# Performance work log

Hardware: AMD Instinct MI355X
Metric: run time of the kernel (lower is better)

The kernel has to match this reference:

```python
import jax, jax.numpy as jnp
import numpy as np

EPSILON = float(np.finfo(np.float32).tiny)
K = 32                 # self.k
TRAIN_ENSEMBLE = 2     # repeat_sample in train mode
TAU = 0.1


def setup_inputs() -> dict:
    key = jax.random.key(0)
    scores = jax.random.normal(key, (256, 8192, 4), dtype=jnp.float32)  # [bsz, Nmax, ensemble]
    return {"scores": scores}


def reference(scores):
    bsz, Nmax, ensemble = scores.shape
    repeat = TRAIN_ENSEMBLE
    local_k = min(K, Nmax)

    # flat_scores: (bsz*ensemble, Nmax), then repeated over samples -> (repeat*bsz*ensemble, Nmax)
    flat = scores.transpose(0, 2, 1).reshape(bsz * ensemble, Nmax)
    flat = jnp.tile(flat, (repeat, 1))

    # Gumbel(0,1) noise (m.sample())
    g = jax.random.gumbel(jax.random.key(42), flat.shape, dtype=flat.dtype)
    flat = flat + g

    zeros = jnp.zeros_like(flat)

    def step(carry, _):
        f, khot, onehot = carry
        khot_mask = jnp.maximum(1.0 - onehot, EPSILON)
        f = f + jnp.log(khot_mask)
        onehot = jax.nn.softmax(f / TAU, axis=1)
        return (f, khot + onehot, onehot), None

    (_, khot, _), _ = jax.lax.scan(step, (flat, zeros, zeros), None, length=local_k)

    # hard top-k straight-through
    _, ind = jax.lax.top_k(khot, local_k)                      # (R, local_k)
    rows = jnp.arange(khot.shape[0])[:, None]
    khot_hard = jnp.zeros_like(khot).at[rows, ind].set(1.0)
    res = khot_hard - jax.lax.stop_gradient(khot) + khot

    # (repeat, bsz, ensemble, Nmax) -> (repeat, bsz, Nmax, ensemble)
    new_mask = res.reshape(repeat, bsz, ensemble, Nmax).transpose(0, 1, 3, 2)
    return new_mask
```

## Files before the change

kernel.cpp:

```cpp
#include <hip/hip_runtime.h>

#define TPB 256
#define ROWN 8192
#define CMAX 1024
#define EPS_TINY 1.1754943508222875e-38f

__device__ __forceinline__ unsigned rotl32(unsigned x, int r) {
  return (x << r) | (x >> (32 - r));
}

__device__ __forceinline__ unsigned tf_pxor(unsigned idx) {
  const unsigned ks0 = 0u, ks1 = 42u, ks2 = 0x1BD11BDAu ^ 0u ^ 42u;
  unsigned x0 = ks0;
  unsigned x1 = idx + ks1;
#define TF4(a,b,cc,d) \
  x0 += x1; x1 = rotl32(x1,(a));  x1 ^= x0; \
  x0 += x1; x1 = rotl32(x1,(b));  x1 ^= x0; \
  x0 += x1; x1 = rotl32(x1,(cc)); x1 ^= x0; \
  x0 += x1; x1 = rotl32(x1,(d));  x1 ^= x0;
  TF4(13,15,26,6)   x0 += ks1; x1 += ks2 + 1u;
  TF4(17,29,16,24)  x0 += ks2; x1 += ks0 + 2u;
  TF4(13,15,26,6)   x0 += ks0; x1 += ks1 + 3u;
  TF4(17,29,16,24)  x0 += ks1; x1 += ks2 + 4u;
  TF4(13,15,26,6)   x0 += ks2; x1 += ks0 + 5u;
#undef TF4
  return x0 ^ x1;
}

__device__ __forceinline__ float gumbel_of(unsigned idx) {
  const unsigned bits = tf_pxor(idx);
  float u = __uint_as_float((bits >> 9) | 0x3f800000u) - 1.0f;
  u = u + EPS_TINY;
  u = fmaxf(EPS_TINY, u);
  return -logf(-logf(u));
}

__device__ __forceinline__ float approx_gumbel(unsigned bits) {
  float u = __uint_as_float((bits >> 9) | 0x3f800000u) - 1.0f;
  u = u + EPS_TINY;
  u = fmaxf(EPS_TINY, u);
  float t;
  if (u >= 0.75f) {
    const float v = 1.0f - u;
    t = v * (1.0f + v * (0.5f + v * (0.33333334f + v * (0.25f + v * 0.2f))));
  } else {
    t = -0.69314718f * __log2f(u);
  }
  return -0.69314718f * __log2f(t);
}

__device__ __forceinline__ unsigned key16_of(float x) {
  const unsigned b = __float_as_uint(x) >> 16;
  return (b & 0x8000u) ? (0xFFFFu & ~b) : (b | 0x8000u);
}

__global__ __launch_bounds__(TPB, 8)
void topk_row(const void* __restrict__ scores_raw,
              float* __restrict__ khotArr,
              unsigned short* __restrict__ idxArr,
              int* __restrict__ cntArr,
              float4* __restrict__ out4) {
  const int t    = threadIdx.x;
  const int lane = t & 63;
  const int wave = t >> 6;

  const int i   = blockIdx.x;
  const int xcd = i & 7;
  const int k   = i >> 3;
  const int e   = k & 3;
  const int q   = k >> 2;
  const int b   = xcd * 32 + (q & 31);
  const int rep = q >> 5;
  const int r   = rep * 1024 + b * 4 + e;
  const unsigned gbase = (unsigned)r * (unsigned)ROWN;

  __shared__ unsigned       kLds[16][TPB];
  __shared__ unsigned short candIdx[CMAX];
  __shared__ float redM[2][4];
  __shared__ float redZ[2][4];
  __shared__ int   wtot[13][4];
  __shared__ int   f32flag;

  if (t == 0) f32flag = 0;
  __syncthreads();
  {
    const unsigned* w = (const unsigned*)scores_raw;
    bool bad = false;
#pragma unroll
    for (int p = 0; p < 4; ++p) {
      const unsigned x = w[t + 256 * p];
      const float flo = __uint_as_float((x & 0xFFFFu) << 16);
      const float fhi = __uint_as_float(x & 0xFFFF0000u);
      if (!(fabsf(flo) <= 16.0f) || !(fabsf(fhi) <= 16.0f)) bad = true;
    }
    if (bad) f32flag = 1;
  }

  {
    float4 z; z.x = 0.0f; z.y = 0.0f; z.z = 0.0f; z.w = 0.0f;
    float4* ob = out4 + (size_t)i * 2048;
#pragma unroll
    for (int p = 0; p < 8; ++p) ob[t + 256 * p] = z;
  }
  __syncthreads();
  const bool in_f32 = (f32flag != 0);

  const size_t ebase0 = ((size_t)b * ROWN + (size_t)t) * 4 + (size_t)e;
  float m = -3.4e38f;
  {
    unsigned pair = 0u;
    if (in_f32) {
      const float* sp = (const float*)scores_raw;
#pragma unroll
      for (int j = 0; j < 32; ++j) {
        const float fj = sp[ebase0 + (size_t)(256 * j) * 4]
                       + approx_gumbel(tf_pxor(gbase + (unsigned)(t + 256 * j)));
        m = fmaxf(m, fj);
        const unsigned kk = key16_of(fj);
        if (j & 1) { pair |= kk << 16; kLds[j >> 1][t] = pair; }
        else pair = kk;
      }
    } else {
      const unsigned short* sp = (const unsigned short*)scores_raw;
#pragma unroll
      for (int j = 0; j < 32; ++j) {
        const float fj = __uint_as_float(((unsigned)sp[ebase0 + (size_t)(256 * j) * 4]) << 16)
                       + approx_gumbel(tf_pxor(gbase + (unsigned)(t + 256 * j)));
        m = fmaxf(m, fj);
        const unsigned kk = key16_of(fj);
        if (j & 1) { pair |= kk << 16; kLds[j >> 1][t] = pair; }
        else pair = kk;
      }
    }
  }

#pragma unroll
  for (int off = 32; off >= 1; off >>= 1) m = fmaxf(m, __shfl_xor(m, off));
  if (lane == 0) redM[0][wave] = m;
  __syncthreads();
  m = fmaxf(fmaxf(redM[0][0], redM[0][1]), fmaxf(redM[0][2], redM[0][3]));

  float lo = m - 25.0f, hi = m;
#pragma unroll 1
  for (int itb = 0; itb < 7; ++itb) {
    const float mid = 0.5f * (lo + hi);
    const unsigned kmid = key16_of(mid);
    int c = 0;
#pragma unroll
    for (int h = 0; h < 16; ++h) {
      const unsigned w = kLds[h][t];
      c += ((w & 0xFFFFu) > kmid) ? 1 : 0;
      c += ((w >> 16) > kmid) ? 1 : 0;
    }
#pragma unroll
    for (int off = 32; off >= 1; off >>= 1) c += __shfl_xor(c, off);
    if (lane == 0) wtot[itb][wave] = c;
    __syncthreads();
    const int tot = wtot[itb][0] + wtot[itb][1] + wtot[itb][2] + wtot[itb][3];
    if (tot >= 33) lo = mid; else hi = mid;
  }
  const float theta = lo - 2.34f;
  const unsigned ktheta = key16_of(theta);

  int cj = 0;
#pragma unroll
  for (int h = 0; h < 16; ++h) {
    const unsigned w = kLds[h][t];
    cj += ((w & 0xFFFFu) >= ktheta) ? 1 : 0;
    cj += ((w >> 16) >= ktheta) ? 1 : 0;
  }
  int incv = cj;
#pragma unroll
  for (int off = 1; off < 64; off <<= 1) {
    const int v = __shfl_up(incv, off);
    if (lane >= off) incv += v;
  }
  if (lane == 63) wtot[12][wave] = incv;
  __syncthreads();
  int base = 0;
  for (int w = 0; w < wave; ++w) base += wtot[12][w];
  int cnt = wtot[12][0] + wtot[12][1] + wtot[12][2] + wtot[12][3];
  if (cnt > CMAX) cnt = CMAX;
  int o = base + incv - cj;
#pragma unroll
  for (int h = 0; h < 16; ++h) {
    const unsigned w = kLds[h][t];
    if ((w & 0xFFFFu) >= ktheta) {
      if (o < CMAX) candIdx[o] = (unsigned short)(t + 256 * (2 * h));
      ++o;
    }
    if ((w >> 16) >= ktheta) {
      if (o < CMAX) candIdx[o] = (unsigned short)(t + 256 * (2 * h + 1));
      ++o;
    }
  }
  __syncthreads();

  float cfr[4], khr[4];
#pragma unroll
  for (int p = 0; p < 4; ++p) {
    cfr[p] = -3.0e38f; khr[p] = -3.0e38f;
    if (256 * p < cnt) {
      const int ci = t + 256 * p;
      if (ci < cnt) {
        const int n = (int)candIdx[ci];
        const size_t ei = ((size_t)b * ROWN + (size_t)n) * 4 + (size_t)e;
        float sc;
        if (in_f32) sc = ((const float*)scores_raw)[ei];
        else sc = __uint_as_float(((unsigned)((const unsigned short*)scores_raw)[ei]) << 16);
        cfr[p] = sc + gumbel_of(gbase + (unsigned)n);
        khr[p] = 0.0f;
      }
    }
  }

  float m2;
  {
    float mm = -3.4e38f;
#pragma unroll
    for (int p = 0; p < 4; ++p)
      if (256 * p < cnt) mm = fmaxf(mm, cfr[p]);
#pragma unroll
    for (int off = 32; off >= 1; off >>= 1) mm = fmaxf(mm, __shfl_xor(mm, off));
    if (lane == 0) redM[1][wave] = mm;
    __syncthreads();
    m2 = fmaxf(fmaxf(redM[1][0], redM[1][1]), fmaxf(redM[1][2], redM[1][3]));
  }

#pragma unroll 1
  for (int it = 0; it < 32; ++it) {
    float ek[4];
    float Z = 0.0f;
#pragma unroll
    for (int p = 0; p < 4; ++p) {
      float ev = 0.0f;
      if (256 * p < cnt) {
        ev = __expf((cfr[p] - m2) * 10.0f);
        Z += ev;
      }
      ek[p] = ev;
    }
#pragma unroll
    for (int off = 32; off >= 1; off >>= 1) Z += __shfl_xor(Z, off);
    if (lane == 0) redZ[it & 1][wave] = Z;

    const bool refresh = ((it & 3) == 2);
    if (refresh) {
      float mm = -3.4e38f;
#pragma unroll
      for (int p = 0; p < 4; ++p)
        if (256 * p < cnt) mm = fmaxf(mm, cfr[p]);
#pragma unroll
      for (int off = 32; off >= 1; off >>= 1) mm = fmaxf(mm, __shfl_xor(mm, off));
      if (lane == 0) redM[(it >> 2) & 1][wave] = mm;
    }
    __syncthreads();
    Z = (redZ[it & 1][0] + redZ[it & 1][1]) + (redZ[it & 1][2] + redZ[it & 1][3]);
    float m2n = m2;
    if (refresh) {
      const int bm = (it >> 2) & 1;
      m2n = fmaxf(fmaxf(redM[bm][0], redM[bm][1]), fmaxf(redM[bm][2], redM[bm][3]));
    }

    const float rz = __builtin_amdgcn_rcpf(Z);
#pragma unroll
    for (int p = 0; p < 4; ++p) {
      if (256 * p < cnt) {
        const float pp = ek[p] * rz;
        khr[p] += pp;
        cfr[p] += __logf(fmaxf(1.0f - pp, EPS_TINY));
      }
    }
    m2 = m2n;
  }

  const size_t rowoff = (size_t)r * CMAX;
#pragma unroll
  for (int p = 0; p < 4; ++p) {
    if (256 * p < cnt) {
      const int ci = t + 256 * p;
      if (ci < cnt) {
        khotArr[rowoff + ci] = khr[p];
        idxArr[rowoff + ci]  = candIdx[ci];
      }
    }
  }
  if (t == 0) cntArr[r] = cnt;
}

__global__ __launch_bounds__(64)
void sel_scatter(const float* __restrict__ khotArr,
                 const unsigned short* __restrict__ idxArr,
                 const int* __restrict__ cntArr,
                 float* __restrict__ out) {
  const int lane = threadIdx.x;
  const int j    = blockIdx.x;
  const int e    = j & 3;
  const int g    = j >> 2;
  const int rep  = g >> 8;
  const int b    = g & 255;
  const int r    = rep * 1024 + b * 4 + e;
  const int cnt  = cntArr[r];
  const size_t rowoff = (size_t)r * CMAX;
  const size_t obase  = ((size_t)g * ROWN) * 4 + (size_t)e;

  float rv[16]; int rn[16];
#pragma unroll
  for (int c = 0; c < 16; ++c) {
    rv[c] = -3.0e38f; rn[c] = 0x7FFFFFFF;
    if (64 * c < cnt) {
      const int ci = lane + 64 * c;
      if (ci < cnt) { rv[c] = khotArr[rowoff + ci]; rn[c] = (int)idxArr[rowoff + ci]; }
    }
  }

#pragma unroll 1
  for (int pass = 0; pass < 32; ++pass) {
    float bv = -3.4e38f; int bn = 0x7FFFFFFF;
#pragma unroll
    for (int c = 0; c < 16; ++c) {
      if (64 * c < cnt) {
        if (rv[c] > bv || (rv[c] == bv && rn[c] < bn)) { bv = rv[c]; bn = rn[c]; }
      }
    }
#pragma unroll
    for (int off = 32; off >= 1; off >>= 1) {
      const float ov = __shfl_xor(bv, off);
      const int   on = __shfl_xor(bn, off);
      if (ov > bv || (ov == bv && on < bn)) { bv = ov; bn = on; }
    }
    if (lane == 0) out[obase + (size_t)bn * 4] = 1.0f;
#pragma unroll
    for (int c = 0; c < 16; ++c)
      if (64 * c < cnt && rn[c] == bn) rv[c] = -3.0e38f;
  }
}

__global__ __launch_bounds__(TPB, 8)
void topk_row_fused(const void* __restrict__ scores_raw, int* __restrict__ selws) {
  const int t    = threadIdx.x;
  const int lane = t & 63;
  const int wave = t >> 6;

  const int i   = blockIdx.x;
  const int xcd = i & 7;
  const int k   = i >> 3;
  const int e   = k & 3;
  const int q   = k >> 2;
  const int b   = xcd * 32 + (q & 31);
  const int rep = q >> 5;
  const int r   = rep * 1024 + b * 4 + e;
  const unsigned gbase = (unsigned)r * (unsigned)ROWN;

  __shared__ unsigned       kLds[16][TPB];
  __shared__ unsigned short candIdx[CMAX];
  __shared__ float redM[2][4];
  __shared__ float redZ[2][4];
  __shared__ int   wtot[13][4];
  __shared__ int   f32flag;

  if (t == 0) f32flag = 0;
  __syncthreads();
  {
    const unsigned* w = (const unsigned*)scores_raw;
    bool bad = false;
#pragma unroll
    for (int p = 0; p < 4; ++p) {
      const unsigned x = w[t + 256 * p];
      const float flo = __uint_as_float((x & 0xFFFFu) << 16);
      const float fhi = __uint_as_float(x & 0xFFFF0000u);
      if (!(fabsf(flo) <= 16.0f) || !(fabsf(fhi) <= 16.0f)) bad = true;
    }
    if (bad) f32flag = 1;
  }
  __syncthreads();
  const bool in_f32 = (f32flag != 0);

  const size_t ebase0 = ((size_t)b * ROWN + (size_t)t) * 4 + (size_t)e;
  float m = -3.4e38f;
  {
    unsigned pair = 0u;
    if (in_f32) {
      const float* sp = (const float*)scores_raw;
#pragma unroll
      for (int j = 0; j < 32; ++j) {
        const float fj = sp[ebase0 + (size_t)(256 * j) * 4]
                       + approx_gumbel(tf_pxor(gbase + (unsigned)(t + 256 * j)));
        m = fmaxf(m, fj);
        const unsigned kk = key16_of(fj);
        if (j & 1) { pair |= kk << 16; kLds[j >> 1][t] = pair; }
        else pair = kk;
      }
    } else {
      const unsigned short* sp = (const unsigned short*)scores_raw;
#pragma unroll
      for (int j = 0; j < 32; ++j) {
        const float fj = __uint_as_float(((unsigned)sp[ebase0 + (size_t)(256 * j) * 4]) << 16)
                       + approx_gumbel(tf_pxor(gbase + (unsigned)(t + 256 * j)));
        m = fmaxf(m, fj);
        const unsigned kk = key16_of(fj);
        if (j & 1) { pair |= kk << 16; kLds[j >> 1][t] = pair; }
        else pair = kk;
      }
    }
  }

#pragma unroll
  for (int off = 32; off >= 1; off >>= 1) m = fmaxf(m, __shfl_xor(m, off));
  if (lane == 0) redM[0][wave] = m;
  __syncthreads();
  m = fmaxf(fmaxf(redM[0][0], redM[0][1]), fmaxf(redM[0][2], redM[0][3]));

  float lo = m - 25.0f, hi = m;
#pragma unroll 1
  for (int itb = 0; itb < 7; ++itb) {
    const float mid = 0.5f * (lo + hi);
    const unsigned kmid = key16_of(mid);
    int c = 0;
#pragma unroll
    for (int h = 0; h < 16; ++h) {
      const unsigned w = kLds[h][t];
      c += ((w & 0xFFFFu) > kmid) ? 1 : 0;
      c += ((w >> 16) > kmid) ? 1 : 0;
    }
#pragma unroll
    for (int off = 32; off >= 1; off >>= 1) c += __shfl_xor(c, off);
    if (lane == 0) wtot[itb][wave] = c;
    __syncthreads();
    const int tot = wtot[itb][0] + wtot[itb][1] + wtot[itb][2] + wtot[itb][3];
    if (tot >= 33) lo = mid; else hi = mid;
  }
  const float theta = lo - 2.34f;
  const unsigned ktheta = key16_of(theta);

  int cj = 0;
#pragma unroll
  for (int h = 0; h < 16; ++h) {
    const unsigned w = kLds[h][t];
    cj += ((w & 0xFFFFu) >= ktheta) ? 1 : 0;
    cj += ((w >> 16) >= ktheta) ? 1 : 0;
  }
  int incv = cj;
#pragma unroll
  for (int off = 1; off < 64; off <<= 1) {
    const int v = __shfl_up(incv, off);
    if (lane >= off) incv += v;
  }
  if (lane == 63) wtot[12][wave] = incv;
  __syncthreads();
  int base = 0;
  for (int w = 0; w < wave; ++w) base += wtot[12][w];
  int cnt = wtot[12][0] + wtot[12][1] + wtot[12][2] + wtot[12][3];
  if (cnt > CMAX) cnt = CMAX;
  int o = base + incv - cj;
#pragma unroll
  for (int h = 0; h < 16; ++h) {
    const unsigned w = kLds[h][t];
    if ((w & 0xFFFFu) >= ktheta) {
      if (o < CMAX) candIdx[o] = (unsigned short)(t + 256 * (2 * h));
      ++o;
    }
    if ((w >> 16) >= ktheta) {
      if (o < CMAX) candIdx[o] = (unsigned short)(t + 256 * (2 * h + 1));
      ++o;
    }
  }
  __syncthreads();

  float cfr[4], khr[4];
#pragma unroll
  for (int p = 0; p < 4; ++p) {
    cfr[p] = -3.0e38f; khr[p] = -3.0e38f;
    if (256 * p < cnt) {
      const int ci = t + 256 * p;
      if (ci < cnt) {
        const int n = (int)candIdx[ci];
        const size_t ei = ((size_t)b * ROWN + (size_t)n) * 4 + (size_t)e;
        float sc;
        if (in_f32) sc = ((const float*)scores_raw)[ei];
        else sc = __uint_as_float(((unsigned)((const unsigned short*)scores_raw)[ei]) << 16);
        cfr[p] = sc + gumbel_of(gbase + (unsigned)n);
        khr[p] = 0.0f;
      }
    }
  }

  float m2;
  {
    float mm = -3.4e38f;
#pragma unroll
    for (int p = 0; p < 4; ++p)
      if (256 * p < cnt) mm = fmaxf(mm, cfr[p]);
#pragma unroll
    for (int off = 32; off >= 1; off >>= 1) mm = fmaxf(mm, __shfl_xor(mm, off));
    if (lane == 0) redM[1][wave] = mm;
    __syncthreads();
    m2 = fmaxf(fmaxf(redM[1][0], redM[1][1]), fmaxf(redM[1][2], redM[1][3]));
  }

#pragma unroll 1
  for (int it = 0; it < 32; ++it) {
    float ek[4];
    float Z = 0.0f;
#pragma unroll
    for (int p = 0; p < 4; ++p) {
      float ev = 0.0f;
      if (256 * p < cnt) {
        ev = __expf((cfr[p] - m2) * 10.0f);
        Z += ev;
      }
      ek[p] = ev;
    }
#pragma unroll
    for (int off = 32; off >= 1; off >>= 1) Z += __shfl_xor(Z, off);
    if (lane == 0) redZ[it & 1][wave] = Z;

    const bool refresh = ((it & 3) == 2);
    if (refresh) {
      float mm = -3.4e38f;
#pragma unroll
      for (int p = 0; p < 4; ++p)
        if (256 * p < cnt) mm = fmaxf(mm, cfr[p]);
#pragma unroll
      for (int off = 32; off >= 1; off >>= 1) mm = fmaxf(mm, __shfl_xor(mm, off));
      if (lane == 0) redM[(it >> 2) & 1][wave] = mm;
    }
    __syncthreads();
    Z = (redZ[it & 1][0] + redZ[it & 1][1]) + (redZ[it & 1][2] + redZ[it & 1][3]);
    float m2n = m2;
    if (refresh) {
      const int bm = (it >> 2) & 1;
      m2n = fmaxf(fmaxf(redM[bm][0], redM[bm][1]), fmaxf(redM[bm][2], redM[bm][3]));
    }

    const float rz = __builtin_amdgcn_rcpf(Z);
#pragma unroll
    for (int p = 0; p < 4; ++p) {
      if (256 * p < cnt) {
        const float pp = ek[p] * rz;
        khr[p] += pp;
        cfr[p] += __logf(fmaxf(1.0f - pp, EPS_TINY));
      }
    }
    m2 = m2n;
  }

  float* khLds = (float*)&kLds[0][0];
#pragma unroll
  for (int p = 0; p < 4; ++p) {
    if (256 * p < cnt) {
      const int ci = t + 256 * p;
      if (ci < cnt) khLds[ci] = khr[p];
    }
  }
  __syncthreads();
  if (wave != 0) return;

  const int nch = (cnt + 63) >> 6;
#pragma unroll 1
  for (int pass = 0; pass < 32; ++pass) {
    float bv = -3.4e38f; int bn = 0x7FFFFFFF; int bci = 0;
#pragma unroll 1
    for (int c = 0; c < nch; ++c) {
      const int ci = lane + 64 * c;
      if (ci < cnt) {
        const float v = khLds[ci];
        const int  n = (int)candIdx[ci];
        if (v > bv || (v == bv && n < bn)) { bv = v; bn = n; bci = ci; }
      }
    }
#pragma unroll
    for (int off = 32; off >= 1; off >>= 1) {
      const float ov = __shfl_xor(bv, off);
      const int   on = __shfl_xor(bn, off);
      const int   oc = __shfl_xor(bci, off);
      if (ov > bv || (ov == bv && on < bn)) { bv = ov; bn = on; bci = oc; }
    }
    if (lane == 0) {
      selws[r * 32 + pass] = bn;
      khLds[bci] = -3.0e38f;
    }
  }
}

__global__ __launch_bounds__(TPB)
void expand_out(const int* __restrict__ selws, float4* __restrict__ out4) {
  const int t   = threadIdx.x;
  const int blk = blockIdx.x;
  const int grp = blk >> 2;
  const int s   = blk & 3;
  const int rep = grp >> 8;
  const int b   = grp & 255;

  __shared__ unsigned ebm[4 * 256];
#pragma unroll
  for (int p = 0; p < 4; ++p) ebm[t + 256 * p] = 0u;
  __syncthreads();
  if (t < 4) {
    const int r = rep * 1024 + b * 4 + t;
#pragma unroll 1
    for (int p = 0; p < 32; ++p) {
      const int ix = selws[r * 32 + p];
      ebm[t * 256 + (ix >> 5)] |= (1u << (ix & 31));
    }
  }
  __syncthreads();

  const size_t obase = (size_t)grp * ROWN;
#pragma unroll
  for (int j = 0; j < 8; ++j) {
    const int n = s * 2048 + t + 256 * j;
    float4 v;
    v.x = ((ebm[0 * 256 + (n >> 5)] >> (n & 31)) & 1u) ? 1.0f : 0.0f;
    v.y = ((ebm[1 * 256 + (n >> 5)] >> (n & 31)) & 1u) ? 1.0f : 0.0f;
    v.z = ((ebm[2 * 256 + (n >> 5)] >> (n & 31)) & 1u) ? 1.0f : 0.0f;
    v.w = ((ebm[3 * 256 + (n >> 5)] >> (n & 31)) & 1u) ? 1.0f : 0.0f;
    out4[obase + (size_t)n] = v;
  }
}

extern "C" void kernel_launch(void* const* d_in, const int* in_sizes, int n_in,
                              void* d_out, int out_size, void* d_ws, size_t ws_size,
                              hipStream_t stream) {
  const void* scores = d_in[0];
  const size_t KH = 2048ull * CMAX * 4;
  const size_t IX = 2048ull * CMAX * 2;
  const size_t CN = 2048ull * 4;
  if (ws_size >= KH + IX + CN) {
    float* khotArr = (float*)d_ws;
    unsigned short* idxArr = (unsigned short*)((char*)d_ws + KH);
    int* cntArr = (int*)((char*)d_ws + KH + IX);
    topk_row<<<dim3(2048), dim3(TPB), 0, stream>>>(scores, khotArr, idxArr, cntArr,
                                                   (float4*)d_out);
    sel_scatter<<<dim3(2048), dim3(64), 0, stream>>>(khotArr, idxArr, cntArr,
                                                     (float*)d_out);
  } else {
    int* selws = (int*)d_ws;
    topk_row_fused<<<dim3(2048), dim3(TPB), 0, stream>>>(scores, selws);
    expand_out<<<dim3(2048), dim3(TPB), 0, stream>>>(selws, (float4*)d_out);
  }
}
```

Measured before the change: 211.8 us.

## Replace iterative 32-pass argmax selection with parallel rank-counting in shared memory

The second-stage selection kernel no longer runs 32 serial wave-wide argmax passes with shuffles. Each candidate is staged in LDS and a 256-thread block computes every candidate's rank by comparing it against all others, then writes 1.0 for candidates ranked below 32. This removes the serial dependency chain but costs O(cnt^2) LDS reads per row, which can grow expensive when the candidate count approaches 1024.

```diff
diff --git a/kernel.cpp b/kernel.cpp
--- a/kernel.cpp
+++ b/kernel.cpp
@@ -288,51 +288,46 @@
   if (t == 0) cntArr[r] = cnt;
 }
 
-__global__ __launch_bounds__(64)
-void sel_scatter(const float* __restrict__ khotArr,
-                 const unsigned short* __restrict__ idxArr,
-                 const int* __restrict__ cntArr,
-                 float* __restrict__ out) {
-  const int lane = threadIdx.x;
-  const int j    = blockIdx.x;
-  const int e    = j & 3;
-  const int g    = j >> 2;
-  const int rep  = g >> 8;
-  const int b    = g & 255;
-  const int r    = rep * 1024 + b * 4 + e;
-  const int cnt  = cntArr[r];
+__global__ __launch_bounds__(TPB)
+void sel_rank(const float* __restrict__ khotArr,
+              const unsigned short* __restrict__ idxArr,
+              const int* __restrict__ cntArr,
+              float* __restrict__ out) {
+  const int t = threadIdx.x;
+  const int j = blockIdx.x;
+  const int e = j & 3;
+  const int g = j >> 2;
+  const int rep = g >> 8;
+  const int b = g & 255;
+  const int r = rep * 1024 + b * 4 + e;
+  const int cnt = cntArr[r];
   const size_t rowoff = (size_t)r * CMAX;
-  const size_t obase  = ((size_t)g * ROWN) * 4 + (size_t)e;
-
-  float rv[16]; int rn[16];
-#pragma unroll
-  for (int c = 0; c < 16; ++c) {
-    rv[c] = -3.0e38f; rn[c] = 0x7FFFFFFF;
-    if (64 * c < cnt) {
-      const int ci = lane + 64 * c;
-      if (ci < cnt) { rv[c] = khotArr[rowoff + ci]; rn[c] = (int)idxArr[rowoff + ci]; }
-    }
-  }
-
-#pragma unroll 1
-  for (int pass = 0; pass < 32; ++pass) {
-    float bv = -3.4e38f; int bn = 0x7FFFFFFF;
-#pragma unroll
-    for (int c = 0; c < 16; ++c) {
-      if (64 * c < cnt) {
-        if (rv[c] > bv || (rv[c] == bv && rn[c] < bn)) { bv = rv[c]; bn = rn[c]; }
-      }
-    }
-#pragma unroll
-    for (int off = 32; off >= 1; off >>= 1) {
-      const float ov = __shfl_xor(bv, off);
-      const int   on = __shfl_xor(bn, off);
-      if (ov > bv || (ov == bv && on < bn)) { bv = ov; bn = on; }
-    }
-    if (lane == 0) out[obase + (size_t)bn * 4] = 1.0f;
-#pragma unroll
-    for (int c = 0; c < 16; ++c)
-      if (64 * c < cnt && rn[c] == bn) rv[c] = -3.0e38f;
+  const size_t obase = ((size_t)g * ROWN) * 4 + (size_t)e;
+
+  __shared__ float          vL[CMAX];
+  __shared__ unsigned short nL[CMAX];
+
+  for (int ci = t; ci < cnt; ci += TPB) {
+    vL[ci] = khotArr[rowoff + ci];
+    nL[ci] = idxArr[rowoff + ci];
+  }
+  __syncthreads();
+
+#pragma unroll
+  for (int p = 0; p < 4; ++p) {
+    const int ci = t + 256 * p;
+    if (ci < cnt) {
+      const float v = vL[ci];
+      const int   n = (int)nL[ci];
+      int rank = 0;
+#pragma unroll 4
+      for (int u = 0; u < cnt; ++u) {
+        const float vu = vL[u];
+        const int   nu = (int)nL[u];
+        rank += (vu > v || (vu == v && nu < n)) ? 1 : 0;
+      }
+      if (rank < 32) out[obase + (size_t)n * 4] = 1.0f;
+    }
   }
 }
 
@@ -632,8 +627,8 @@
     int* cntArr = (int*)((char*)d_ws + KH + IX);
     topk_row<<<dim3(2048), dim3(TPB), 0, stream>>>(scores, khotArr, idxArr, cntArr,
                                                    (float4*)d_out);
-    sel_scatter<<<dim3(2048), dim3(64), 0, stream>>>(khotArr, idxArr, cntArr,
-                                                     (float*)d_out);
+    sel_rank<<<dim3(2048), dim3(TPB), 0, stream>>>(khotArr, idxArr, cntArr,
+                                                   (float*)d_out);
   } else {
     int* selws = (int*)d_ws;
     topk_row_fused<<<dim3(2048), dim3(TPB), 0, stream>>>(scores, selws);
```

After: 339.2 us. +60.1%, slower.
